# Kernel tuning notes

Hardware: AMD Instinct MI355X
Metric: run time of the kernel (lower is better)

## Reference

```python
import jax, jax.numpy as jnp
import numpy as np

N_HEAD = 16
N_KV = 4
HEAD_DIM = 128
EPS = float(np.finfo(np.float32).eps)  # torch F.rms_norm default eps


def _rope_tables(T, half, dtype=jnp.float32):
    inv_freq = 1.0 / (10000.0 ** (jnp.arange(half, dtype=dtype) / half))
    ang = jnp.arange(T, dtype=dtype)[:, None] * inv_freq[None, :]  # (T, half)
    cos = jnp.cos(ang)[None, :, None, :]  # (1, T, 1, half)
    sin = jnp.sin(ang)[None, :, None, :]
    return cos, sin


def setup_inputs() -> dict:
    key = jax.random.key(0)
    ks = jax.random.split(key, 5)
    B, T, C = 2, 2048, 2048
    x = jax.random.normal(ks[0], (B, T, C), dtype=jnp.float32)
    cos, sin = _rope_tables(T, HEAD_DIM // 2)
    s = 0.02
    W_Q = jax.random.normal(ks[1], (C, N_HEAD * HEAD_DIM), dtype=jnp.float32) * s
    W_K = jax.random.normal(ks[2], (C, N_KV * HEAD_DIM), dtype=jnp.float32) * s
    W_V = jax.random.normal(ks[3], (C, N_KV * HEAD_DIM), dtype=jnp.float32) * s
    W_O = jax.random.normal(ks[4], (C, C), dtype=jnp.float32) * s
    return {"x": x, "cos": cos, "sin": sin, "W_Q": W_Q, "W_K": W_K, "W_V": W_V, "W_O": W_O}


def _apply_rope(x, cos, sin):
    # x: (B,T,H,D); cos/sin: (1,T,1,D/2)
    d = x.shape[-1] // 2
    x1, x2 = x[..., :d], x[..., d:]
    return jnp.concatenate([x1 * cos + x2 * sin, -x1 * sin + x2 * cos], axis=-1)


def _rms_norm(x):
    return x * jax.lax.rsqrt(jnp.mean(x * x, axis=-1, keepdims=True) + EPS)


def reference(x, cos, sin, W_Q, W_K, W_V, W_O):
    B, T, C = x.shape
    G = N_HEAD // N_KV  # kv groups
    q = (x @ W_Q).reshape(B, T, N_HEAD, HEAD_DIM)
    k = (x @ W_K).reshape(B, T, N_KV, HEAD_DIM)
    v = (x @ W_V).reshape(B, T, N_KV, HEAD_DIM)
    q = _rms_norm(_apply_rope(q, cos[:, :T], sin[:, :T]))
    k = _rms_norm(_apply_rope(k, cos[:, :T], sin[:, :T]))
    # GQA: avoid materializing expanded K/V; group q by kv head
    qg = q.reshape(B, T, N_KV, G, HEAD_DIM)
    scale = 1.0 / jnp.sqrt(jnp.asarray(HEAD_DIM, dtype=x.dtype))
    scores = jnp.einsum("btkgd,bskd->bkgts", qg, k) * scale  # (B,Kv,G,T,T)
    causal = jnp.tril(jnp.ones((T, T), dtype=bool))
    scores = jnp.where(causal, scores, jnp.asarray(-jnp.inf, dtype=scores.dtype))
    attn = jax.nn.softmax(scores, axis=-1)
    out = jnp.einsum("bkgts,bskd->btkgd", attn, v).reshape(B, T, C)
    return out @ W_O
```

## Files before the change

### kernel.cpp

```cpp
#include <hip/hip_runtime.h>
#include <hip/hip_bf16.h>
#include <stdint.h>

typedef __bf16 bf16_4 __attribute__((ext_vector_type(4)));
typedef __bf16 bf16_8 __attribute__((ext_vector_type(8)));
typedef float f32x4 __attribute__((ext_vector_type(4)));

#define AS1 __attribute__((address_space(1)))
#define AS3 __attribute__((address_space(3)))

__device__ __forceinline__ void gload_lds16(const void* g, void* l) {
  __builtin_amdgcn_global_load_lds((const AS1 void*)g, (AS3 void*)l, 16, 0, 0);
}

__global__ void detect_dtype(const void* __restrict__ cosT, int* __restrict__ flag) {
  uint32_t w = *reinterpret_cast<const uint32_t*>(cosT);
  *flag = ((w & 0xFFFFu) == 0x3F80u) ? 1 : 0;
}

__global__ __launch_bounds__(256) void to_bf16_vec(const void* __restrict__ src,
                                                   __bf16* __restrict__ dst,
                                                   int n8, const int* __restrict__ flag) {
  const int i = blockIdx.x * 256 + threadIdx.x;
  if (i >= n8) return;
  if (*flag) {
    reinterpret_cast<int4*>(dst)[i] = reinterpret_cast<const int4*>(src)[i];
  } else {
    const float4* s = reinterpret_cast<const float4*>(src);
    const float4 a = s[2 * i], b = s[2 * i + 1];
    __bf16 o[8] = {(__bf16)a.x, (__bf16)a.y, (__bf16)a.z, (__bf16)a.w,
                   (__bf16)b.x, (__bf16)b.y, (__bf16)b.z, (__bf16)b.w};
    reinterpret_cast<int4*>(dst)[i] = *reinterpret_cast<int4*>(o);
  }
}

__global__ __launch_bounds__(256) void tables_to_f32(const void* __restrict__ c,
                                                     const void* __restrict__ s,
                                                     float* __restrict__ dst, int n,
                                                     const int* __restrict__ flag) {
  const int i = blockIdx.x * 256 + threadIdx.x;
  if (i >= n) return;
  if (*flag) {
    dst[i]     = (float)reinterpret_cast<const __bf16*>(c)[i];
    dst[n + i] = (float)reinterpret_cast<const __bf16*>(s)[i];
  } else {
    dst[i]     = reinterpret_cast<const float*>(c)[i];
    dst[n + i] = reinterpret_cast<const float*>(s)[i];
  }
}

__global__ void transpose_all(const void* __restrict__ WQ, const void* __restrict__ WK,
                              const void* __restrict__ WV, const void* __restrict__ WO,
                              __bf16* __restrict__ Wt, __bf16* __restrict__ WOt,
                              const int* __restrict__ flag) {
  __shared__ __bf16 t[32][33];
  const int bx = blockIdx.x;
  const void* src;
  __bf16* dst;
  int C, c0;
  if (bx < 64)      { src = WQ; dst = Wt;                          C = 2048; c0 = bx * 32; }
  else if (bx < 80) { src = WK; dst = Wt + (size_t)2048 * 2048;    C = 512;  c0 = (bx - 64) * 32; }
  else if (bx < 96) { src = WV; dst = Wt + (size_t)2560 * 2048;    C = 512;  c0 = (bx - 80) * 32; }
  else              { src = WO; dst = WOt;                         C = 2048; c0 = (bx - 96) * 32; }
  const int r0 = blockIdx.y * 32;
  const bool isb = (*flag != 0);
  #pragma unroll
  for (int i = 0; i < 32; i += 8) {
    const size_t idx = (size_t)(r0 + threadIdx.y + i) * C + c0 + threadIdx.x;
    t[threadIdx.y + i][threadIdx.x] =
        isb ? reinterpret_cast<const __bf16*>(src)[idx]
            : (__bf16)reinterpret_cast<const float*>(src)[idx];
  }
  __syncthreads();
  #pragma unroll
  for (int i = 0; i < 32; i += 8)
    dst[(size_t)(c0 + threadIdx.y + i) * 2048 + r0 + threadIdx.x] = t[threadIdx.x][threadIdx.y + i];
}

__global__ void vtrans(const __bf16* __restrict__ qkv, __bf16* __restrict__ vt) {
  __shared__ __bf16 t[32][33];
  const int b = blockIdx.z;
  const int t0 = blockIdx.x * 32, c0 = blockIdx.y * 32;
  #pragma unroll
  for (int i = 0; i < 32; i += 8)
    t[threadIdx.y + i][threadIdx.x] =
        qkv[(size_t)(b * 2048 + t0 + threadIdx.y + i) * 3072 + 2560 + c0 + threadIdx.x];
  __syncthreads();
  #pragma unroll
  for (int i = 0; i < 32; i += 8)
    vt[(size_t)(b * 512 + c0 + threadIdx.y + i) * 2048 + t0 + threadIdx.x] =
        t[threadIdx.x][threadIdx.y + i];
}

template <int DYN>
__global__ __launch_bounds__(512) void gemm8p(const __bf16* __restrict__ A,
                                              const __bf16* __restrict__ Bt,
                                              void* __restrict__ Cv,
                                              int M, int N, int K,
                                              const int* __restrict__ flag) {
  __shared__ __attribute__((aligned(16))) __bf16 As[2][128 * 64];
  __shared__ __attribute__((aligned(16))) __bf16 Bs[2][256 * 64];
  const int tid = threadIdx.x;
  const int lane = tid & 63, w = tid >> 6;
  const int wm = w >> 2, wn = w & 3;
  const int r = lane & 15, g = lane >> 4;
  const int bm = blockIdx.x * 128, bn = blockIdx.y * 256;
  const bool isb = DYN ? (*flag != 0) : true;
  const int NT = K >> 6;

  f32x4 acc[4][4] = {};

#define STA(kt, p, j)                                                              \
  {                                                                                \
    const int o_ = tid * 16 + (j) * 8192;                                          \
    const int row_ = o_ >> 7, blk_ = (o_ >> 4) & 7;                                \
    gload_lds16(A + (size_t)(bm + row_) * K + (kt) * 64 + ((blk_ ^ (row_ & 7)) << 3), \
                (char*)As[p] + o_);                                                \
  }
#define STB(kt, p, j)                                                              \
  {                                                                                \
    const int o_ = tid * 16 + (j) * 8192;                                          \
    const int rl_ = o_ >> 7, blk_ = (o_ >> 4) & 7;                                 \
    const int gr_ = ((rl_ >> 5) & 3) * 64 + ((rl_ >> 7) & 1) * 32 + (rl_ & 31);    \
    gload_lds16(Bt + (size_t)(bn + gr_) * K + (kt) * 64 + ((blk_ ^ (rl_ & 7)) << 3), \
                (char*)Bs[p] + o_);                                                \
  }

  STA(0, 0, 0); STA(0, 0, 1);
  STB(0, 0, 0); STB(0, 0, 1); STB(0, 0, 2); STB(0, 0, 3);
  asm volatile("s_waitcnt vmcnt(2)\ns_barrier" ::: "memory");

  for (int kt = 0; kt < NT; ++kt) {
    const int cur = kt & 1, nxt = cur ^ 1;
    const bool pf = (kt + 1 < NT);
    const char* Ac = (const char*)As[cur];
    const char* Bc = (const char*)Bs[cur];

    bf16_8 af[4][2], bf[2][2];
    #pragma unroll
    for (int m = 0; m < 4; ++m)
      #pragma unroll
      for (int kk = 0; kk < 2; ++kk) {
        const int row = wm * 64 + m * 16 + r;
        af[m][kk] = *reinterpret_cast<const bf16_8*>(
            Ac + row * 128 + (((kk * 4 + g) ^ (row & 7)) << 4));
      }
    #pragma unroll
    for (int n = 0; n < 2; ++n)
      #pragma unroll
      for (int kk = 0; kk < 2; ++kk) {
        const int rl = wn * 32 + n * 16 + r;
        bf[n][kk] = *reinterpret_cast<const bf16_8*>(
            Bc + rl * 128 + (((kk * 4 + g) ^ (rl & 7)) << 4));
      }
    if (pf) { STA(kt + 1, nxt, 0); STA(kt + 1, nxt, 1); STB(kt + 1, nxt, 0); }
    __builtin_amdgcn_s_barrier();
    __builtin_amdgcn_s_setprio(1);
    #pragma unroll
    for (int kk = 0; kk < 2; ++kk)
      #pragma unroll
      for (int m = 0; m < 4; ++m)
        #pragma unroll
        for (int n = 0; n < 2; ++n)
          acc[m][n] = __builtin_amdgcn_mfma_f32_16x16x32_bf16(af[m][kk], bf[n][kk], acc[m][n], 0, 0, 0);
    __builtin_amdgcn_s_setprio(0);
    if (pf) asm volatile("s_waitcnt vmcnt(3)\ns_barrier" ::: "memory");
    else    asm volatile("s_waitcnt vmcnt(0)\ns_barrier" ::: "memory");

    bf16_8 bg[2][2];
    #pragma unroll
    for (int n = 0; n < 2; ++n)
      #pragma unroll
      for (int kk = 0; kk < 2; ++kk) {
        const int rl = 128 + wn * 32 + n * 16 + r;
        bg[n][kk] = *reinterpret_cast<const bf16_8*>(
            Bc + rl * 128 + (((kk * 4 + g) ^ (rl & 7)) << 4));
      }
    if (pf) { STB(kt + 1, nxt, 1); STB(kt + 1, nxt, 2); STB(kt + 1, nxt, 3); }
    __builtin_amdgcn_s_barrier();
    __builtin_amdgcn_s_setprio(1);
    #pragma unroll
    for (int kk = 0; kk < 2; ++kk)
      #pragma unroll
      for (int m = 0; m < 4; ++m)
        #pragma unroll
        for (int n = 0; n < 2; ++n)
          acc[m][n + 2] = __builtin_amdgcn_mfma_f32_16x16x32_bf16(af[m][kk], bg[n][kk], acc[m][n + 2], 0, 0, 0);
    __builtin_amdgcn_s_setprio(0);
    if (pf) asm volatile("s_waitcnt vmcnt(2)\ns_barrier" ::: "memory");
    else    asm volatile("s_waitcnt vmcnt(0)\ns_barrier" ::: "memory");
  }
#undef STA
#undef STB

  #pragma unroll
  for (int m = 0; m < 4; ++m)
    #pragma unroll
    for (int n = 0; n < 4; ++n)
      #pragma unroll
      for (int j = 0; j < 4; ++j) {
        const int row = bm + wm * 64 + m * 16 + g * 4 + j;
        const int col = bn + wn * 64 + n * 16 + r;
        const float v = acc[m][n][j];
        if (isb) reinterpret_cast<__bf16*>(Cv)[(size_t)row * N + col] = (__bf16)v;
        else     reinterpret_cast<float*>(Cv)[(size_t)row * N + col] = v;
      }
}

__global__ __launch_bounds__(256) void rope_rms(__bf16* __restrict__ qkv,
                                                const float* __restrict__ csF) {
  const int gw = blockIdx.x * 4 + (threadIdx.x >> 6);
  const int lane = threadIdx.x & 63;
  const int head = gw % 20;
  const int m = gw / 20;
  const int t = m & 2047;
  __bf16* p = qkv + (size_t)m * 3072 + head * 128;
  const float x1 = (float)p[lane];
  const float x2 = (float)p[lane + 64];
  const float c = csF[t * 64 + lane];
  const float s = csF[131072 + t * 64 + lane];
  const float y1 = x1 * c + x2 * s;
  const float y2 = x2 * c - x1 * s;
  float ss = y1 * y1 + y2 * y2;
  #pragma unroll
  for (int mk = 32; mk >= 1; mk >>= 1) ss += __shfl_xor(ss, mk, 64);
  float inv = rsqrtf(ss * (1.0f / 128.0f) + 1.1920929e-7f);
  if (head < 16) inv *= 0.12751743f;
  p[lane] = (__bf16)(y1 * inv);
  p[lane + 64] = (__bf16)(y2 * inv);
}

__global__ __launch_bounds__(256) void attn_fwd7(const __bf16* __restrict__ qkv,
                                                 const __bf16* __restrict__ vt,
                                                 __bf16* __restrict__ out) {
  __shared__ __attribute__((aligned(16))) __bf16 Kl[64 * 128];
  __shared__ __attribute__((aligned(16))) __bf16 Vl[128 * 64];
  __shared__ __attribute__((aligned(16))) __bf16 Pl[4][16][64];

  const int tid = threadIdx.x, lane = tid & 63, w = tid >> 6;
  const int r = lane & 15, g = lane >> 4;
  const int lid = blockIdx.x;
  const int grp = lid & 7, inner = lid >> 3;
  const int b = grp >> 2, kvh = grp & 3;
  const int h = kvh * 4 + (inner & 3);
  const int qt = 31 - (inner >> 2);
  const int nt = qt + 1;
  const __bf16* Kbase = qkv + (size_t)(b * 2048) * 3072 + 2048 + kvh * 128;
  const __bf16* Vbase = vt + (size_t)((b * 4 + kvh) * 128) * 2048;

#define STAGE(kt)                                                               \
  {                                                                             \
    _Pragma("unroll")                                                           \
    for (int i_ = 0; i_ < 4; ++i_) {                                            \
      const int o_ = tid * 16 + i_ * 4096;                                      \
      const int krow_ = o_ >> 8;                                                \
      const int jj_ = (o_ >> 4) & 15;                                           \
      const int gj_ = (jj_ & 8) | ((jj_ ^ krow_) & 7);                          \
      gload_lds16(Kbase + (size_t)((kt) * 64 + krow_) * 3072 + gj_ * 8,         \
                  (char*)Kl + o_);                                              \
      const int d_ = o_ >> 7;                                                   \
      const int j2_ = (o_ >> 4) & 7;                                            \
      const int g2_ = j2_ ^ (d_ & 7);                                           \
      gload_lds16(Vbase + (size_t)d_ * 2048 + (kt) * 64 + g2_ * 8,              \
                  (char*)Vl + o_);                                              \
    }                                                                           \
  }

  bf16_8 qf[4];
  {
    const __bf16* qp = qkv + (size_t)(b * 2048 + qt * 64 + w * 16 + r) * 3072 + h * 128 + g * 8;
    #pragma unroll
    for (int kb = 0; kb < 4; ++kb) qf[kb] = *reinterpret_cast<const bf16_8*>(qp + kb * 32);
  }

  char* const plw = (char*)Pl + w * 2048;
  f32x4 accO[8] = {};
  float mst = -1e30f, lst = 0.0f;

  for (int kt = 0; kt < nt; ++kt) {
    STAGE(kt);
    asm volatile("s_waitcnt vmcnt(0)" ::: "memory");
    __syncthreads();

    f32x4 sacc[4] = {};
    #pragma unroll
    for (int kb = 0; kb < 4; ++kb) {
      const int jj = kb * 4 + g;
      const int jp = (jj & 8) | ((jj ^ (r & 7)) & 7);
      #pragma unroll
      for (int n = 0; n < 4; ++n) {
        const bf16_8 kf = *reinterpret_cast<const bf16_8*>((char*)Kl + (n * 16 + r) * 256 + jp * 16);
        sacc[n] = __builtin_amdgcn_mfma_f32_16x16x32_bf16(kf, qf[kb], sacc[n], 0, 0, 0);
      }
    }

    float p[4][4];
    float pm = -1e30f;
    #pragma unroll
    for (int n = 0; n < 4; ++n)
      #pragma unroll
      for (int j = 0; j < 4; ++j) {
        p[n][j] = sacc[n][j];
        pm = fmaxf(pm, p[n][j]);
      }
    if (kt == qt) {
      const int qpos = qt * 64 + w * 16 + r;
      pm = -1e30f;
      #pragma unroll
      for (int n = 0; n < 4; ++n)
        #pragma unroll
        for (int j = 0; j < 4; ++j) {
          if (kt * 64 + n * 16 + g * 4 + j > qpos) p[n][j] = -1e30f;
          pm = fmaxf(pm, p[n][j]);
        }
    }
    pm = fmaxf(pm, __shfl_xor(pm, 16, 64));
    pm = fmaxf(pm, __shfl_xor(pm, 32, 64));

    float mn = mst;
    if (!__all(pm - mst <= 12.0f)) {
      mn = fmaxf(mst, pm);
      const float alpha = exp2f(mst - mn);
      mst = mn;
      lst *= alpha;
      float av[4];
      #pragma unroll
      for (int j = 0; j < 4; ++j) av[j] = __shfl(alpha, g * 4 + j, 64);
      #pragma unroll
      for (int dt = 0; dt < 8; ++dt)
        #pragma unroll
        for (int j = 0; j < 4; ++j) accO[dt][j] *= av[j];
    }
    float rs = 0.0f;
    #pragma unroll
    for (int n = 0; n < 4; ++n)
      #pragma unroll
      for (int j = 0; j < 4; ++j) {
        p[n][j] = exp2f(p[n][j] - mn);
        rs += p[n][j];
      }
    rs += __shfl_xor(rs, 16, 64);
    rs += __shfl_xor(rs, 32, 64);
    lst += rs;

    #pragma unroll
    for (int n = 0; n < 4; ++n) {
      bf16_4 pk;
      #pragma unroll
      for (int j = 0; j < 4; ++j) pk[j] = (__bf16)p[n][j];
      const int blk = 2 * n + (g >> 1);
      char* pw = plw + r * 128 + ((blk ^ (r & 7)) << 4) + (g & 1) * 8;
      *reinterpret_cast<bf16_4*>(pw) = pk;
    }

    #pragma unroll
    for (int half = 0; half < 2; ++half) {
      const bf16_8 pa = *reinterpret_cast<const bf16_8*>(
          plw + r * 128 + (((half * 4 + g) ^ (r & 7)) << 4));
      #pragma unroll
      for (int dt = 0; dt < 8; ++dt) {
        const int d = dt * 16 + r;
        const bf16_8 vf = *reinterpret_cast<const bf16_8*>((char*)Vl + d * 128 + ((half * 4 + g) ^ (d & 7)) * 16);
        accO[dt] = __builtin_amdgcn_mfma_f32_16x16x32_bf16(pa, vf, accO[dt], 0, 0, 0);
      }
    }

    __syncthreads();
  }

  float lv[4];
  #pragma unroll
  for (int j = 0; j < 4; ++j) lv[j] = 1.0f / __shfl(lst, g * 4 + j, 64);
  #pragma unroll
  for (int dt = 0; dt < 8; ++dt)
    #pragma unroll
    for (int j = 0; j < 4; ++j) {
      const int t = qt * 64 + w * 16 + g * 4 + j;
      out[(size_t)(b * 2048 + t) * 2048 + h * 128 + dt * 16 + r] = (__bf16)(accO[dt][j] * lv[j]);
    }
#undef STAGE
}

extern "C" void kernel_launch(void* const* d_in, const int* in_sizes, int n_in,
                              void* d_out, int out_size, void* d_ws, size_t ws_size,
                              hipStream_t stream) {
  const void* x    = d_in[0];
  const void* cosT = d_in[1];
  const void* sinT = d_in[2];
  const void* W_Q  = d_in[3];
  const void* W_K  = d_in[4];
  const void* W_V  = d_in[5];
  const void* W_O  = d_in[6];

  const int B = 2, T = 2048, C = 2048;
  const int M = B * T;
  const int NQKV = 3072;

  char* ws = (char*)d_ws;
  int*    flag = (int*)ws;                       ws += 256;
  float*  csF  = (float*)ws;                     ws += (size_t)2 * 131072 * 4;
  __bf16* xb   = (__bf16*)ws;                    ws += (size_t)M * C * 2;
  __bf16* Wt   = (__bf16*)ws;                    ws += (size_t)NQKV * C * 2;
  __bf16* WOt  = (__bf16*)ws;                    ws += (size_t)C * C * 2;
  __bf16* QKV  = (__bf16*)ws;                    ws += (size_t)M * NQKV * 2;
  __bf16* AO   = (__bf16*)ws;                    ws += (size_t)M * C * 2;
  __bf16* VT   = xb;

  detect_dtype<<<1, 1, 0, stream>>>(cosT, flag);
  tables_to_f32<<<131072 / 256, 256, 0, stream>>>(cosT, sinT, csF, 131072, flag);
  to_bf16_vec<<<(M * C / 8) / 256, 256, 0, stream>>>(x, xb, M * C / 8, flag);

  transpose_all<<<dim3(160, 64), dim3(32, 8), 0, stream>>>(W_Q, W_K, W_V, W_O, Wt, WOt, flag);

  gemm8p<0><<<dim3(M / 128, NQKV / 256), 512, 0, stream>>>(xb, Wt, QKV, M, NQKV, C, flag);
  rope_rms<<<dim3(M * 20 / 4), 256, 0, stream>>>(QKV, csF);
  vtrans<<<dim3(T / 32, 512 / 32, B), dim3(32, 8), 0, stream>>>(QKV, VT);
  attn_fwd7<<<dim3(1024), 256, 0, stream>>>(QKV, VT, AO);
  gemm8p<1><<<dim3(M / 128, C / 256), 512, 0, stream>>>(AO, WOt, d_out, M, C, C, flag);
}
```

Before: 227.9 us.

## Replace LDS-staged attention with single-wave blocks loading K/V from global

Result: slower. 403.1 us (+76.8%).

```diff
diff --git a/kernel.cpp b/kernel.cpp
--- a/kernel.cpp
+++ b/kernel.cpp
@@ -230,69 +230,45 @@
   p[lane + 64] = (__bf16)(y2 * inv);
 }
 
-__global__ __launch_bounds__(256) void attn_fwd7(const __bf16* __restrict__ qkv,
-                                                 const __bf16* __restrict__ vt,
-                                                 __bf16* __restrict__ out) {
-  __shared__ __attribute__((aligned(16))) __bf16 Kl[64 * 128];
-  __shared__ __attribute__((aligned(16))) __bf16 Vl[128 * 64];
-  __shared__ __attribute__((aligned(16))) __bf16 Pl[4][16][64];
-
-  const int tid = threadIdx.x, lane = tid & 63, w = tid >> 6;
+__global__ __launch_bounds__(64) void attn_fwd8(const __bf16* __restrict__ qkv,
+                                                const __bf16* __restrict__ vt,
+                                                __bf16* __restrict__ out) {
+  __shared__ __attribute__((aligned(16))) __bf16 Pl[16][64];
+
+  const int lane = threadIdx.x;
   const int r = lane & 15, g = lane >> 4;
   const int lid = blockIdx.x;
   const int grp = lid & 7, inner = lid >> 3;
   const int b = grp >> 2, kvh = grp & 3;
   const int h = kvh * 4 + (inner & 3);
-  const int qt = 31 - (inner >> 2);
+  const int rem = inner >> 2;
+  const int qt = 31 - (rem >> 2);
+  const int w4 = rem & 3;
+  const int qrow0 = qt * 64 + w4 * 16;
   const int nt = qt + 1;
   const __bf16* Kbase = qkv + (size_t)(b * 2048) * 3072 + 2048 + kvh * 128;
   const __bf16* Vbase = vt + (size_t)((b * 4 + kvh) * 128) * 2048;
 
-#define STAGE(kt)                                                               \
-  {                                                                             \
-    _Pragma("unroll")                                                           \
-    for (int i_ = 0; i_ < 4; ++i_) {                                            \
-      const int o_ = tid * 16 + i_ * 4096;                                      \
-      const int krow_ = o_ >> 8;                                                \
-      const int jj_ = (o_ >> 4) & 15;                                           \
-      const int gj_ = (jj_ & 8) | ((jj_ ^ krow_) & 7);                          \
-      gload_lds16(Kbase + (size_t)((kt) * 64 + krow_) * 3072 + gj_ * 8,         \
-                  (char*)Kl + o_);                                              \
-      const int d_ = o_ >> 7;                                                   \
-      const int j2_ = (o_ >> 4) & 7;                                            \
-      const int g2_ = j2_ ^ (d_ & 7);                                           \
-      gload_lds16(Vbase + (size_t)d_ * 2048 + (kt) * 64 + g2_ * 8,              \
-                  (char*)Vl + o_);                                              \
-    }                                                                           \
-  }
-
   bf16_8 qf[4];
   {
-    const __bf16* qp = qkv + (size_t)(b * 2048 + qt * 64 + w * 16 + r) * 3072 + h * 128 + g * 8;
+    const __bf16* qp = qkv + (size_t)(b * 2048 + qrow0 + r) * 3072 + h * 128 + g * 8;
     #pragma unroll
     for (int kb = 0; kb < 4; ++kb) qf[kb] = *reinterpret_cast<const bf16_8*>(qp + kb * 32);
   }
 
-  char* const plw = (char*)Pl + w * 2048;
   f32x4 accO[8] = {};
   float mst = -1e30f, lst = 0.0f;
 
   for (int kt = 0; kt < nt; ++kt) {
-    STAGE(kt);
-    asm volatile("s_waitcnt vmcnt(0)" ::: "memory");
-    __syncthreads();
-
     f32x4 sacc[4] = {};
     #pragma unroll
-    for (int kb = 0; kb < 4; ++kb) {
-      const int jj = kb * 4 + g;
-      const int jp = (jj & 8) | ((jj ^ (r & 7)) & 7);
+    for (int kb = 0; kb < 4; ++kb)
       #pragma unroll
       for (int n = 0; n < 4; ++n) {
-        const bf16_8 kf = *reinterpret_cast<const bf16_8*>((char*)Kl + (n * 16 + r) * 256 + jp * 16);
+        const bf16_8 kf = *reinterpret_cast<const bf16_8*>(
+            Kbase + (size_t)(kt * 64 + n * 16 + r) * 3072 + kb * 32 + g * 8);
         sacc[n] = __builtin_amdgcn_mfma_f32_16x16x32_bf16(kf, qf[kb], sacc[n], 0, 0, 0);
       }
-    }
 
     float p[4][4];
     float pm = -1e30f;
@@ -304,7 +280,7 @@
         pm = fmaxf(pm, p[n][j]);
       }
     if (kt == qt) {
-      const int qpos = qt * 64 + w * 16 + r;
+      const int qpos = qrow0 + r;
       pm = -1e30f;
       #pragma unroll
       for (int n = 0; n < 4; ++n)
@@ -349,23 +325,22 @@
       #pragma unroll
       for (int j = 0; j < 4; ++j) pk[j] = (__bf16)p[n][j];
       const int blk = 2 * n + (g >> 1);
-      char* pw = plw + r * 128 + ((blk ^ (r & 7)) << 4) + (g & 1) * 8;
+      char* pw = (char*)Pl + r * 128 + ((blk ^ (r & 7)) << 4) + (g & 1) * 8;
       *reinterpret_cast<bf16_4*>(pw) = pk;
     }
 
     #pragma unroll
     for (int half = 0; half < 2; ++half) {
       const bf16_8 pa = *reinterpret_cast<const bf16_8*>(
-          plw + r * 128 + (((half * 4 + g) ^ (r & 7)) << 4));
+          (char*)Pl + r * 128 + (((half * 4 + g) ^ (r & 7)) << 4));
       #pragma unroll
       for (int dt = 0; dt < 8; ++dt) {
         const int d = dt * 16 + r;
-        const bf16_8 vf = *reinterpret_cast<const bf16_8*>((char*)Vl + d * 128 + ((half * 4 + g) ^ (d & 7)) * 16);
+        const bf16_8 vf = *reinterpret_cast<const bf16_8*>(
+            Vbase + (size_t)d * 2048 + kt * 64 + half * 32 + g * 8);
         accO[dt] = __builtin_amdgcn_mfma_f32_16x16x32_bf16(pa, vf, accO[dt], 0, 0, 0);
       }
     }
-
-    __syncthreads();
   }
 
   float lv[4];
@@ -375,10 +350,9 @@
   for (int dt = 0; dt < 8; ++dt)
     #pragma unroll
     for (int j = 0; j < 4; ++j) {
-      const int t = qt * 64 + w * 16 + g * 4 + j;
+      const int t = qrow0 + g * 4 + j;
       out[(size_t)(b * 2048 + t) * 2048 + h * 128 + dt * 16 + r] = (__bf16)(accO[dt][j] * lv[j]);
     }
-#undef STAGE
 }
 
 extern "C" void kernel_launch(void* const* d_in, const int* in_sizes, int n_in,
@@ -415,6 +389,6 @@
   gemm8p<0><<<dim3(M / 128, NQKV / 256), 512, 0, stream>>>(xb, Wt, QKV, M, NQKV, C, flag);
   rope_rms<<<dim3(M * 20 / 4), 256, 0, stream>>>(QKV, csF);
   vtrans<<<dim3(T / 32, 512 / 32, B), dim3(32, 8), 0, stream>>>(QKV, VT);
-  attn_fwd7<<<dim3(1024), 256, 0, stream>>>(QKV, VT, AO);
+  attn_fwd8<<<dim3(4096), 64, 0, stream>>>(QKV, VT, AO);
   gemm8p<1><<<dim3(M / 128, C / 256), 512, 0, stream>>>(AO, WOt, d_out, M, C, C, flag);
 }
```

## Merge prep and rope/V-transpose kernels; swizzle GEMM block order across XCDs

Applied to the files above, without the earlier changes.

Result: no change. 229.2 us (+0.6%).

```diff
diff --git a/kernel.cpp b/kernel.cpp
--- a/kernel.cpp
+++ b/kernel.cpp
@@ -18,78 +18,66 @@
   *flag = ((w & 0xFFFFu) == 0x3F80u) ? 1 : 0;
 }
 
-__global__ __launch_bounds__(256) void to_bf16_vec(const void* __restrict__ src,
-                                                   __bf16* __restrict__ dst,
-                                                   int n8, const int* __restrict__ flag) {
-  const int i = blockIdx.x * 256 + threadIdx.x;
-  if (i >= n8) return;
-  if (*flag) {
-    reinterpret_cast<int4*>(dst)[i] = reinterpret_cast<const int4*>(src)[i];
-  } else {
-    const float4* s = reinterpret_cast<const float4*>(src);
-    const float4 a = s[2 * i], b = s[2 * i + 1];
-    __bf16 o[8] = {(__bf16)a.x, (__bf16)a.y, (__bf16)a.z, (__bf16)a.w,
-                   (__bf16)b.x, (__bf16)b.y, (__bf16)b.z, (__bf16)b.w};
-    reinterpret_cast<int4*>(dst)[i] = *reinterpret_cast<int4*>(o);
-  }
-}
-
-__global__ __launch_bounds__(256) void tables_to_f32(const void* __restrict__ c,
-                                                     const void* __restrict__ s,
-                                                     float* __restrict__ dst, int n,
-                                                     const int* __restrict__ flag) {
-  const int i = blockIdx.x * 256 + threadIdx.x;
-  if (i >= n) return;
-  if (*flag) {
-    dst[i]     = (float)reinterpret_cast<const __bf16*>(c)[i];
-    dst[n + i] = (float)reinterpret_cast<const __bf16*>(s)[i];
-  } else {
-    dst[i]     = reinterpret_cast<const float*>(c)[i];
-    dst[n + i] = reinterpret_cast<const float*>(s)[i];
-  }
-}
-
-__global__ void transpose_all(const void* __restrict__ WQ, const void* __restrict__ WK,
-                              const void* __restrict__ WV, const void* __restrict__ WO,
-                              __bf16* __restrict__ Wt, __bf16* __restrict__ WOt,
-                              const int* __restrict__ flag) {
+__global__ __launch_bounds__(256) void prep_all(const void* __restrict__ cosT,
+                                                const void* __restrict__ sinT,
+                                                const void* __restrict__ x,
+                                                const void* __restrict__ WQ,
+                                                const void* __restrict__ WK,
+                                                const void* __restrict__ WV,
+                                                const void* __restrict__ WO,
+                                                float* __restrict__ csF,
+                                                __bf16* __restrict__ xb,
+                                                __bf16* __restrict__ Wt,
+                                                __bf16* __restrict__ WOt,
+                                                const int* __restrict__ flag) {
+  const int blk = blockIdx.x, tid = threadIdx.x;
+  const bool isb = (*flag != 0);
+  if (blk < 512) {
+    const int i = blk * 256 + tid;
+    if (isb) {
+      csF[i]          = (float)reinterpret_cast<const __bf16*>(cosT)[i];
+      csF[131072 + i] = (float)reinterpret_cast<const __bf16*>(sinT)[i];
+    } else {
+      csF[i]          = reinterpret_cast<const float*>(cosT)[i];
+      csF[131072 + i] = reinterpret_cast<const float*>(sinT)[i];
+    }
+    return;
+  }
+  if (blk < 4608) {
+    const int i = (blk - 512) * 256 + tid;
+    if (isb) {
+      reinterpret_cast<int4*>(xb)[i] = reinterpret_cast<const int4*>(x)[i];
+    } else {
+      const float4* s = reinterpret_cast<const float4*>(x);
+      const float4 a = s[2 * i], c = s[2 * i + 1];
+      __bf16 o[8] = {(__bf16)a.x, (__bf16)a.y, (__bf16)a.z, (__bf16)a.w,
+                     (__bf16)c.x, (__bf16)c.y, (__bf16)c.z, (__bf16)c.w};
+      reinterpret_cast<int4*>(xb)[i] = *reinterpret_cast<int4*>(o);
+    }
+    return;
+  }
   __shared__ __bf16 t[32][33];
-  const int bx = blockIdx.x;
+  const int tb = blk - 4608;
+  const int bx = tb % 160, by = tb / 160;
+  const int tx = tid & 31, ty = tid >> 5;
   const void* src;
   __bf16* dst;
   int C, c0;
-  if (bx < 64)      { src = WQ; dst = Wt;                          C = 2048; c0 = bx * 32; }
-  else if (bx < 80) { src = WK; dst = Wt + (size_t)2048 * 2048;    C = 512;  c0 = (bx - 64) * 32; }
-  else if (bx < 96) { src = WV; dst = Wt + (size_t)2560 * 2048;    C = 512;  c0 = (bx - 80) * 32; }
-  else              { src = WO; dst = WOt;                         C = 2048; c0 = (bx - 96) * 32; }
-  const int r0 = blockIdx.y * 32;
-  const bool isb = (*flag != 0);
+  if (bx < 64)      { src = WQ; dst = Wt;                        C = 2048; c0 = bx * 32; }
+  else if (bx < 80) { src = WK; dst = Wt + (size_t)2048 * 2048;  C = 512;  c0 = (bx - 64) * 32; }
+  else if (bx < 96) { src = WV; dst = Wt + (size_t)2560 * 2048;  C = 512;  c0 = (bx - 80) * 32; }
+  else              { src = WO; dst = WOt;                       C = 2048; c0 = (bx - 96) * 32; }
+  const int r0 = by * 32;
   #pragma unroll
   for (int i = 0; i < 32; i += 8) {
-    const size_t idx = (size_t)(r0 + threadIdx.y + i) * C + c0 + threadIdx.x;
-    t[threadIdx.y + i][threadIdx.x] =
-        isb ? reinterpret_cast<const __bf16*>(src)[idx]
-            : (__bf16)reinterpret_cast<const float*>(src)[idx];
+    const size_t idx = (size_t)(r0 + ty + i) * C + c0 + tx;
+    t[ty + i][tx] = isb ? reinterpret_cast<const __bf16*>(src)[idx]
+                        : (__bf16)reinterpret_cast<const float*>(src)[idx];
   }
   __syncthreads();
   #pragma unroll
   for (int i = 0; i < 32; i += 8)
-    dst[(size_t)(c0 + threadIdx.y + i) * 2048 + r0 + threadIdx.x] = t[threadIdx.x][threadIdx.y + i];
-}
-
-__global__ void vtrans(const __bf16* __restrict__ qkv, __bf16* __restrict__ vt) {
-  __shared__ __bf16 t[32][33];
-  const int b = blockIdx.z;
-  const int t0 = blockIdx.x * 32, c0 = blockIdx.y * 32;
-  #pragma unroll
-  for (int i = 0; i < 32; i += 8)
-    t[threadIdx.y + i][threadIdx.x] =
-        qkv[(size_t)(b * 2048 + t0 + threadIdx.y + i) * 3072 + 2560 + c0 + threadIdx.x];
-  __syncthreads();
-  #pragma unroll
-  for (int i = 0; i < 32; i += 8)
-    vt[(size_t)(b * 512 + c0 + threadIdx.y + i) * 2048 + t0 + threadIdx.x] =
-        t[threadIdx.x][threadIdx.y + i];
+    dst[(size_t)(c0 + ty + i) * 2048 + r0 + tx] = t[tx][ty + i];
 }
 
 template <int DYN>
@@ -104,7 +92,10 @@
   const int lane = tid & 63, w = tid >> 6;
   const int wm = w >> 2, wn = w & 3;
   const int r = lane & 15, g = lane >> 4;
-  const int bm = blockIdx.x * 128, bn = blockIdx.y * 256;
+  const int q8 = gridDim.x >> 3;
+  const int wg = (blockIdx.x & 7) * q8 + (blockIdx.x >> 3);
+  const int gx = M >> 7;
+  const int bm = (wg % gx) * 128, bn = (wg / gx) * 256;
   const bool isb = DYN ? (*flag != 0) : true;
   const int NT = K >> 6;
 
@@ -207,27 +198,45 @@
       }
 }
 
-__global__ __launch_bounds__(256) void rope_rms(__bf16* __restrict__ qkv,
-                                                const float* __restrict__ csF) {
-  const int gw = blockIdx.x * 4 + (threadIdx.x >> 6);
-  const int lane = threadIdx.x & 63;
-  const int head = gw % 20;
-  const int m = gw / 20;
-  const int t = m & 2047;
-  __bf16* p = qkv + (size_t)m * 3072 + head * 128;
-  const float x1 = (float)p[lane];
-  const float x2 = (float)p[lane + 64];
-  const float c = csF[t * 64 + lane];
-  const float s = csF[131072 + t * 64 + lane];
-  const float y1 = x1 * c + x2 * s;
-  const float y2 = x2 * c - x1 * s;
-  float ss = y1 * y1 + y2 * y2;
-  #pragma unroll
-  for (int mk = 32; mk >= 1; mk >>= 1) ss += __shfl_xor(ss, mk, 64);
-  float inv = rsqrtf(ss * (1.0f / 128.0f) + 1.1920929e-7f);
-  if (head < 16) inv *= 0.12751743f;
-  p[lane] = (__bf16)(y1 * inv);
-  p[lane + 64] = (__bf16)(y2 * inv);
+__global__ __launch_bounds__(256) void rope_vtrans(__bf16* __restrict__ qkv,
+                                                   const float* __restrict__ csF,
+                                                   __bf16* __restrict__ vt) {
+  const int blk = blockIdx.x, tid = threadIdx.x;
+  if (blk < 20480) {
+    const int gw = blk * 4 + (tid >> 6);
+    const int lane = tid & 63;
+    const int head = gw % 20;
+    const int m = gw / 20;
+    const int t = m & 2047;
+    __bf16* p = qkv + (size_t)m * 3072 + head * 128;
+    const float x1 = (float)p[lane];
+    const float x2 = (float)p[lane + 64];
+    const float c = csF[t * 64 + lane];
+    const float s = csF[131072 + t * 64 + lane];
+    const float y1 = x1 * c + x2 * s;
+    const float y2 = x2 * c - x1 * s;
+    float ss = y1 * y1 + y2 * y2;
+    #pragma unroll
+    for (int mk = 32; mk >= 1; mk >>= 1) ss += __shfl_xor(ss, mk, 64);
+    float inv = rsqrtf(ss * (1.0f / 128.0f) + 1.1920929e-7f);
+    if (head < 16) inv *= 0.12751743f;
+    p[lane] = (__bf16)(y1 * inv);
+    p[lane + 64] = (__bf16)(y2 * inv);
+    return;
+  }
+  __shared__ __bf16 t[32][33];
+  const int vb = blk - 20480;
+  const int z = vb >> 10, rem = vb & 1023;
+  const int x = rem & 63, y = rem >> 6;
+  const int tx = tid & 31, ty = tid >> 5;
+  const int t0 = x * 32, c0 = y * 32;
+  #pragma unroll
+  for (int i = 0; i < 32; i += 8)
+    t[ty + i][tx] = qkv[(size_t)(z * 2048 + t0 + ty + i) * 3072 + 2560 + c0 + tx];
+  __syncthreads();
+  #pragma unroll
+  for (int i = 0; i < 32; i += 8)
+    vt[(size_t)(z * 512 + c0 + ty + i) * 2048 + t0 + tx] = t[tx][ty + i];
 }
 
 __global__ __launch_bounds__(256) void attn_fwd7(const __bf16* __restrict__ qkv,
@@ -407,14 +416,10 @@
   __bf16* VT   = xb;
 
   detect_dtype<<<1, 1, 0, stream>>>(cosT, flag);
-  tables_to_f32<<<131072 / 256, 256, 0, stream>>>(cosT, sinT, csF, 131072, flag);
-  to_bf16_vec<<<(M * C / 8) / 256, 256, 0, stream>>>(x, xb, M * C / 8, flag);
-
-  transpose_all<<<dim3(160, 64), dim3(32, 8), 0, stream>>>(W_Q, W_K, W_V, W_O, Wt, WOt, flag);
-
-  gemm8p<0><<<dim3(M / 128, NQKV / 256), 512, 0, stream>>>(xb, Wt, QKV, M, NQKV, C, flag);
-  rope_rms<<<dim3(M * 20 / 4), 256, 0, stream>>>(QKV, csF);
-  vtrans<<<dim3(T / 32, 512 / 32, B), dim3(32, 8), 0, stream>>>(QKV, VT);
+  prep_all<<<dim3(14848), 256, 0, stream>>>(cosT, sinT, x, W_Q, W_K, W_V, W_O,
+                                            csF, xb, Wt, WOt, flag);
+  gemm8p<0><<<dim3((M / 128) * (NQKV / 256)), 512, 0, stream>>>(xb, Wt, QKV, M, NQKV, C, flag);
+  rope_vtrans<<<dim3(22528), 256, 0, stream>>>(QKV, csF, VT);
   attn_fwd7<<<dim3(1024), 256, 0, stream>>>(QKV, VT, AO);
-  gemm8p<1><<<dim3(M / 128, C / 256), 512, 0, stream>>>(AO, WOt, d_out, M, C, C, flag);
-}
+  gemm8p<1><<<dim3((M / 128) * (C / 256)), 512, 0, stream>>>(AO, WOt, d_out, M, C, C, flag);
+}
```
